# Optimization experiments

Measured on AMD Instinct MI355X. Metric: run time of the kernel, lower is better.

Reference implementation:

```python
import jax, jax.numpy as jnp
import numpy as np

N = 50000      # nodes
E = 1000000    # edges
B = 512        # graphs in batch
F = 32         # num_node_features
D = 64         # hidden_dim1
ED = 16        # edge_dim (8 edge_attr + 8 edge_feature)
STEPS = 3      # set2set processing steps


def setup_inputs() -> dict:
    key = jax.random.key(0)
    ks = jax.random.split(key, 24)
    rn = lambda k, shp, s=0.05: jax.random.normal(k, shp, dtype=jnp.float32) * s
    z = lambda *shp: jnp.zeros(shp, jnp.float32)
    inp = {}
    inp["x"] = jax.random.normal(ks[0], (N, F), dtype=jnp.float32)
    inp["edge_attr"] = jax.random.normal(ks[1], (E, 8), dtype=jnp.float32)
    inp["edge_feature"] = jax.random.normal(ks[2], (E, 8), dtype=jnp.float32)
    inp["edge_index"] = jax.random.randint(ks[3], (2, E), 0, N, dtype=jnp.int32)
    inp["batch"] = jnp.sort(jax.random.randint(ks[4], (N,), 0, B, dtype=jnp.int32))
    # conv0: GINEConv with nn = Linear(F,D)-ReLU-Linear(D,D); edge lin: ED -> F
    inp["conv0_ew"] = rn(ks[5], (ED, F)); inp["conv0_eb"] = z(F)
    inp["conv0_w1"] = rn(ks[6], (F, D));  inp["conv0_b1"] = z(D)
    inp["conv0_w2"] = rn(ks[7], (D, D));  inp["conv0_b2"] = z(D)
    # conv1: nn = Linear(D,D)-ReLU-Linear(D,D); edge lin: ED -> D
    inp["conv1_ew"] = rn(ks[8], (ED, D)); inp["conv1_eb"] = z(D)
    inp["conv1_w1"] = rn(ks[9], (D, D));  inp["conv1_b1"] = z(D)
    inp["conv1_w2"] = rn(ks[10], (D, D)); inp["conv1_b2"] = z(D)
    # Set2Set LSTM: input 2D -> hidden D (torch gate order i,f,g,o)
    inp["lstm_wih"] = rn(ks[11], (4 * D, 2 * D)); inp["lstm_bih"] = z(4 * D)
    inp["lstm_whh"] = rn(ks[12], (4 * D, D));     inp["lstm_bhh"] = z(4 * D)
    # dense head
    inp["dense_w"] = rn(ks[13], (2 * D, D)); inp["dense_b"] = z(D)
    inp["out_w"] = rn(ks[14], (D, 1));       inp["out_b"] = z(1)
    return inp


def _gine_conv(x, src, dst, eattr, ew, eb, w1, b1, w2, b2):
    # message = relu(x_j + lin(edge_attr)); sum-aggregate at target; eps=0
    msg = jax.nn.relu(x[src] + eattr @ ew + eb)          # [E, C]
    agg = jax.ops.segment_sum(msg, dst, num_segments=N)   # [N, C]
    h = x + agg                                            # (1+eps)*x + agg, eps=0
    return jax.nn.relu(h @ w1 + b1) @ w2 + b2


def _set2set(x, batch, wih, whh, bih, bhh):
    d = x.shape[1]
    q_star = jnp.zeros((B, 2 * d), x.dtype)
    h = jnp.zeros((B, d), x.dtype)
    c = jnp.zeros((B, d), x.dtype)
    for _ in range(STEPS):
        gates = q_star @ wih.T + bih + h @ whh.T + bhh     # [B, 4d]
        i, f, g, o = jnp.split(gates, 4, axis=1)
        c = jax.nn.sigmoid(f) * c + jax.nn.sigmoid(i) * jnp.tanh(g)
        h = jax.nn.sigmoid(o) * jnp.tanh(c)
        q = h                                              # [B, d]
        e = jnp.sum(x * q[batch], axis=-1)                 # [N]
        m = jax.ops.segment_max(e, batch, num_segments=B)
        ex = jnp.exp(e - m[batch])
        denom = jax.ops.segment_sum(ex, batch, num_segments=B)
        a = ex / denom[batch]                              # segmented softmax
        r = jax.ops.segment_sum(a[:, None] * x, batch, num_segments=B)  # [B, d]
        q_star = jnp.concatenate([q, r], axis=-1)
    return q_star


def reference(x, edge_attr, edge_feature, edge_index, batch,
              conv0_ew, conv0_eb, conv0_w1, conv0_b1, conv0_w2, conv0_b2,
              conv1_ew, conv1_eb, conv1_w1, conv1_b1, conv1_w2, conv1_b2,
              lstm_wih, lstm_whh, lstm_bih, lstm_bhh,
              dense_w, dense_b, out_w, out_b):
    ea = jnp.concatenate([edge_attr, edge_feature], axis=1)  # [E, ED]
    src, dst = edge_index[0], edge_index[1]
    h = jax.nn.relu(_gine_conv(x, src, dst, ea, conv0_ew, conv0_eb,
                               conv0_w1, conv0_b1, conv0_w2, conv0_b2))
    h = jax.nn.relu(_gine_conv(h, src, dst, ea, conv1_ew, conv1_eb,
                               conv1_w1, conv1_b1, conv1_w2, conv1_b2))
    pooled = _set2set(h, batch, lstm_wih, lstm_whh, lstm_bih, lstm_bhh)  # [B, 2D]
    z = jax.nn.relu(pooled @ dense_w + dense_b)
    return (z @ out_w + out_b)[:, 0]
```

## Files before the change

### kernel.cpp

```cpp
#include <hip/hip_runtime.h>
#include <math.h>

#define NN 50000
#define EE 1000000
#define BB 512

typedef _Float16 hf;
typedef __attribute__((ext_vector_type(2))) _Float16 hf2;

__device__ __forceinline__ float sigmoidf_(float x) { return 1.0f / (1.0f + __expf(-x)); }

__device__ __forceinline__ int uloadi(const int* p) {
    return __builtin_amdgcn_readfirstlane(*p);
}
__device__ __forceinline__ unsigned uloadu(const unsigned* p) {
    return (unsigned)__builtin_amdgcn_readfirstlane((int)*p);
}

__device__ __forceinline__ unsigned pack2(float a, float b) {
    hf2 h; h.x = (_Float16)a; h.y = (_Float16)b;
    return __builtin_bit_cast(unsigned, h);
}

__device__ __forceinline__ float dot2acc(unsigned au, hf2 w, float acc) {
    hf2 a = __builtin_bit_cast(hf2, au);
#if __has_builtin(__builtin_amdgcn_fdot2)
    return __builtin_amdgcn_fdot2(a, w, acc, false);
#else
    return acc + (float)a.x * (float)w.x + (float)a.y * (float)w.y;
#endif
}

__global__ __launch_bounds__(256) void setup_kernel(
    const int* __restrict__ batch, int* __restrict__ brow,
    const float* __restrict__ wih, const float* __restrict__ whh,
    float* __restrict__ wihT, float* __restrict__ whhT,
    int* __restrict__ counts, const float* __restrict__ x, unsigned* __restrict__ xh)
{
    int i = blockIdx.x * 256 + threadIdx.x;
    if (i < NN) {
        counts[i] = 0;
        int bi = batch[i];
        int prev = (i == 0) ? -1 : batch[i - 1];
        for (int v = prev + 1; v <= bi; ++v) brow[v] = i;
        if (i == NN - 1) for (int v = bi + 1; v <= BB; ++v) brow[v] = NN;
    }
    if (i < 128 * 256) wihT[i] = wih[(i & 255) * 128 + (i >> 8)];
    if (i < 64 * 256)  whhT[i] = whh[(i & 255) * 64 + (i >> 8)];
    if (i < NN * 8) {
        float4 v = reinterpret_cast<const float4*>(x)[i];
        uint2 o; o.x = pack2(v.x, v.y); o.y = pack2(v.z, v.w);
        reinterpret_cast<uint2*>(xh)[i] = o;
    }
}

__global__ __launch_bounds__(256) void rank_kernel(const int* __restrict__ ei,
                                                   int* __restrict__ counts,
                                                   int* __restrict__ rnk)
{
    int e = blockIdx.x * 256 + threadIdx.x;
    if (e < EE) rnk[e] = atomicAdd(&counts[ei[EE + e]], 1);
}

__global__ __launch_bounds__(1024) void scan_kernel(const int* __restrict__ counts,
                                                    int* __restrict__ rowptr)
{
    __shared__ int s[1024];
    int t = threadIdx.x;
    const int CH = (NN + 1023) / 1024;
    int lo = t * CH, hi = lo + CH < NN ? lo + CH : NN;
    int sum = 0;
    for (int i = lo; i < hi; ++i) sum += counts[i];
    s[t] = sum;
    __syncthreads();
    for (int off = 1; off < 1024; off <<= 1) {
        int v = (t >= off) ? s[t - off] : 0;
        __syncthreads();
        s[t] += v;
        __syncthreads();
    }
    int base = (t > 0) ? s[t - 1] : 0;
    for (int i = lo; i < hi; ++i) { rowptr[i] = base; base += counts[i]; }
    if (t == 1023) rowptr[NN] = s[1023];
}

__global__ __launch_bounds__(256) void pack_kernel(
    const int* __restrict__ ei, const int* __restrict__ rnk,
    const int* __restrict__ rowptr,
    const float* __restrict__ eattr, const float* __restrict__ efeat,
    int* __restrict__ srcp, unsigned* __restrict__ eah)
{
    int e = blockIdx.x * 256 + threadIdx.x;
    if (e >= EE) return;
    int pos = rowptr[ei[EE + e]] + rnk[e];
    srcp[pos] = ei[e];
    const float4* pa = reinterpret_cast<const float4*>(eattr) + (size_t)e * 2;
    const float4* pf = reinterpret_cast<const float4*>(efeat) + (size_t)e * 2;
    float4 v0 = pa[0], v1 = pa[1], v2 = pf[0], v3 = pf[1];
    uint4 o0, o1;
    o0.x = pack2(v0.x, v0.y); o0.y = pack2(v0.z, v0.w);
    o0.z = pack2(v1.x, v1.y); o0.w = pack2(v1.z, v1.w);
    o1.x = pack2(v2.x, v2.y); o1.y = pack2(v2.z, v2.w);
    o1.z = pack2(v3.x, v3.y); o1.w = pack2(v3.z, v3.w);
    uint4* o = reinterpret_cast<uint4*>(eah + (size_t)pos * 8);
    o[0] = o0; o[1] = o1;
}

__global__ __launch_bounds__(256) void gine32_kernel(
    const hf* __restrict__ xin, const int* __restrict__ pidx,
    const int* __restrict__ rowptr, const unsigned* __restrict__ eah,
    const float* __restrict__ ew, const float* __restrict__ eb,
    const float* __restrict__ w1, const float* __restrict__ b1,
    const float* __restrict__ w2, const float* __restrict__ b2,
    hf* __restrict__ hout)
{
    __shared__ float w1_lds[32 * 64];
    for (int i = threadIdx.x; i < 32 * 64; i += 256) w1_lds[i] = w1[i];
    __syncthreads();

    int wave = threadIdx.x >> 6, lane = threadIdx.x & 63;
    int node = blockIdx.x * 4 + wave;
    if (node >= NN) return;

    int ch = lane & 31;
    int half = lane >> 5;

    hf2 wh[8];
#pragma unroll
    for (int k = 0; k < 8; ++k) {
        wh[k].x = (_Float16)ew[(2 * k) * 32 + ch];
        wh[k].y = (_Float16)ew[(2 * k + 1) * 32 + ch];
    }
    float ebv = eb[ch];

    int start = rowptr[node], end = rowptr[node + 1];
    float agg = 0.0f;

    int j = start;
    for (; j + 1 < end; j += 2) {
        int jb = __builtin_amdgcn_readfirstlane(j);
        int s0 = uloadi(pidx + jb);
        int s1 = uloadi(pidx + jb + 1);
        float xv = (float)xin[(size_t)(half ? s1 : s0) * 32 + ch];
        const unsigned* p = eah + (size_t)jb * 8;
        unsigned a0[8], a1[8];
#pragma unroll
        for (int k = 0; k < 8; ++k) { a0[k] = uloadu(p + k); a1[k] = uloadu(p + 8 + k); }
        float m0 = 0.0f, m1 = 0.0f;
#pragma unroll
        for (int k = 0; k < 8; ++k) {
            m0 = dot2acc(a0[k], wh[k], m0);
            m1 = dot2acc(a1[k], wh[k], m1);
        }
        agg += fmaxf(xv + (half ? m1 : m0) + ebv, 0.0f);
    }
    if (j < end) {
        int jb = __builtin_amdgcn_readfirstlane(j);
        int s0 = uloadi(pidx + jb);
        float xv = (float)xin[(size_t)s0 * 32 + ch];
        const unsigned* p = eah + (size_t)jb * 8;
        float m0 = 0.0f;
#pragma unroll
        for (int k = 0; k < 8; ++k) m0 = dot2acc(uloadu(p + k), wh[k], m0);
        agg += (half == 0) ? fmaxf(xv + m0 + ebv, 0.0f) : 0.0f;
    }
    agg += __shfl_xor(agg, 32);

    float h_in = 0.0f;
    if (lane < 32) h_in = (float)xin[(size_t)node * 32 + lane] + agg;

    float hid = b1[lane];
#pragma unroll
    for (int i = 0; i < 32; ++i)
        hid += __shfl(h_in, i) * w1_lds[i * 64 + lane];
    hid = fmaxf(hid, 0.0f);

    float o = b2[lane];
#pragma unroll
    for (int i = 0; i < 64; ++i)
        o += __shfl(hid, i) * w2[i * 64 + lane];

    hout[(size_t)node * 64 + lane] = (hf)fmaxf(o, 0.0f);
}

__global__ __launch_bounds__(256) void gine64_kernel(
    const hf* __restrict__ xin, const int* __restrict__ pidx,
    const int* __restrict__ rowptr, const unsigned* __restrict__ eah,
    const float* __restrict__ ew, const float* __restrict__ eb,
    const float* __restrict__ w1, const float* __restrict__ b1,
    const float* __restrict__ w2, const float* __restrict__ b2,
    hf* __restrict__ hout)
{
    __shared__ float w1_lds[64 * 64];
    for (int i = threadIdx.x; i < 64 * 64; i += 256) w1_lds[i] = w1[i];
    __syncthreads();

    int wave = threadIdx.x >> 6, lane = threadIdx.x & 63;
    int node = blockIdx.x * 4 + wave;
    if (node >= NN) return;

    int ch32 = lane & 31;
    int half = lane >> 5;
    int start = rowptr[node], end = rowptr[node + 1];

    auto run_pass = [&](int cb) -> float {
        int c = cb + ch32;
        hf2 wh[8];
#pragma unroll
        for (int k = 0; k < 8; ++k) {
            wh[k].x = (_Float16)ew[(2 * k) * 64 + c];
            wh[k].y = (_Float16)ew[(2 * k + 1) * 64 + c];
        }
        float ebv = eb[c];
        float agg = 0.0f;
        int j = start;
        for (; j + 1 < end; j += 2) {
            int jb = __builtin_amdgcn_readfirstlane(j);
            int s0 = uloadi(pidx + jb);
            int s1 = uloadi(pidx + jb + 1);
            float xv = (float)xin[(size_t)(half ? s1 : s0) * 64 + c];
            const unsigned* p = eah + (size_t)jb * 8;
            unsigned a0[8], a1[8];
#pragma unroll
            for (int k = 0; k < 8; ++k) { a0[k] = uloadu(p + k); a1[k] = uloadu(p + 8 + k); }
            float m0 = 0.0f, m1 = 0.0f;
#pragma unroll
            for (int k = 0; k < 8; ++k) {
                m0 = dot2acc(a0[k], wh[k], m0);
                m1 = dot2acc(a1[k], wh[k], m1);
            }
            agg += fmaxf(xv + (half ? m1 : m0) + ebv, 0.0f);
        }
        if (j < end) {
            int jb = __builtin_amdgcn_readfirstlane(j);
            int s0 = uloadi(pidx + jb);
            float xv = (float)xin[(size_t)s0 * 64 + c];
            const unsigned* p = eah + (size_t)jb * 8;
            float m0 = 0.0f;
#pragma unroll
            for (int k = 0; k < 8; ++k) m0 = dot2acc(uloadu(p + k), wh[k], m0);
            agg += (half == 0) ? fmaxf(xv + m0 + ebv, 0.0f) : 0.0f;
        }
        agg += __shfl_xor(agg, 32);
        return agg;
    };

    float agg_lo = run_pass(0);
    float agg_hi = run_pass(32);

    float h_in = (float)xin[(size_t)node * 64 + lane]
               + ((lane < 32) ? agg_lo : agg_hi);

    float hid = b1[lane];
#pragma unroll
    for (int i = 0; i < 64; ++i)
        hid += __shfl(h_in, i) * w1_lds[i * 64 + lane];
    hid = fmaxf(hid, 0.0f);

    float o = b2[lane];
#pragma unroll
    for (int i = 0; i < 64; ++i)
        o += __shfl(hid, i) * w2[i * 64 + lane];

    hout[(size_t)node * 64 + lane] = (hf)fmaxf(o, 0.0f);
}

__global__ __launch_bounds__(1024) void set2set_head_v3(
    const hf* __restrict__ h2, const int* __restrict__ brow,
    const float* __restrict__ wihT, const float* __restrict__ whhT,
    const float* __restrict__ bih, const float* __restrict__ bhh,
    const float* __restrict__ dw, const float* __restrict__ db,
    const float* __restrict__ ow, const float* __restrict__ ob,
    float* __restrict__ outp)
{
    int b = blockIdx.x, tid = threadIdx.x;
    int wv = tid >> 6, lane = tid & 63;
    __shared__ float qstar[128], hh[64], cc[64];
    __shared__ float gpart[4][256];
    __shared__ float redw[16][64];
    __shared__ float redm[16], reds[16];

    int start = brow[b], end = brow[b + 1];

    if (tid < 128) qstar[tid] = 0.0f;
    if (tid < 64) { hh[tid] = 0.0f; cc[tid] = 0.0f; }
    __syncthreads();

    for (int step = 0; step < 3; ++step) {
        {
            int p = tid >> 8, g = tid & 255;
            float acc = 0.0f;
            const float* wT = wihT + (size_t)(32 * p) * 256 + g;
#pragma unroll 8
            for (int k = 0; k < 32; ++k) acc += qstar[32 * p + k] * wT[(size_t)k * 256];
            const float* hT = whhT + (size_t)(16 * p) * 256 + g;
#pragma unroll 8
            for (int k = 0; k < 16; ++k) acc += hh[16 * p + k] * hT[(size_t)k * 256];
            gpart[p][g] = acc;
        }
        __syncthreads();
        if (tid < 64) {
            float gi = bih[tid]       + bhh[tid]       + gpart[0][tid]       + gpart[1][tid]       + gpart[2][tid]       + gpart[3][tid];
            float gf = bih[64 + tid]  + bhh[64 + tid]  + gpart[0][64 + tid]  + gpart[1][64 + tid]  + gpart[2][64 + tid]  + gpart[3][64 + tid];
            float gg = bih[128 + tid] + bhh[128 + tid] + gpart[0][128 + tid] + gpart[1][128 + tid] + gpart[2][128 + tid] + gpart[3][128 + tid];
            float go = bih[192 + tid] + bhh[192 + tid] + gpart[0][192 + tid] + gpart[1][192 + tid] + gpart[2][192 + tid] + gpart[3][192 + tid];
            float c = sigmoidf_(gf) * cc[tid] + sigmoidf_(gi) * tanhf(gg);
            cc[tid] = c;
            hh[tid] = sigmoidf_(go) * tanhf(c);
        }
        __syncthreads();

        float qv = hh[lane];
        float mw = -INFINITY, sw = 0.0f, rw = 0.0f;
        for (int n = start + wv; n < end; n += 16) {
            float v = (float)h2[(size_t)n * 64 + lane];
            float p = v * qv;
#pragma unroll
            for (int off = 32; off; off >>= 1) p += __shfl_xor(p, off);
            float nm = fmaxf(mw, p);
            float sc = __expf(mw - nm);
            float pe = __expf(p - nm);
            sw = sw * sc + pe;
            rw = rw * sc + pe * v;
            mw = nm;
        }
        redm[wv] = mw; reds[wv] = sw; redw[wv][lane] = rw;
        __syncthreads();
        if (tid < 64) {
            float M = -INFINITY;
#pragma unroll
            for (int w = 0; w < 16; ++w) M = fmaxf(M, redm[w]);
            float S = 0.0f, R = 0.0f;
#pragma unroll
            for (int w = 0; w < 16; ++w) {
                float mm = redm[w];
                if (mm > -INFINITY) {
                    float sc = __expf(mm - M);
                    S += reds[w] * sc;
                    R += redw[w][tid] * sc;
                }
            }
            qstar[tid] = hh[tid];
            qstar[64 + tid] = (S > 0.0f) ? R / S : 0.0f;
        }
        __syncthreads();
    }

    if (tid < 64) {
        float z = db[tid];
#pragma unroll 4
        for (int k = 0; k < 128; ++k) z += qstar[k] * dw[k * 64 + tid];
        redw[0][tid] = fmaxf(z, 0.0f);
    }
    __syncthreads();
    if (tid < 64) {
        float t = redw[0][tid] * ow[tid];
#pragma unroll
        for (int off = 32; off; off >>= 1) t += __shfl_xor(t, off);
        if (tid == 0) outp[b] = t + ob[0];
    }
}

extern "C" void kernel_launch(void* const* d_in, const int* in_sizes, int n_in,
                              void* d_out, int out_size, void* d_ws, size_t ws_size,
                              hipStream_t stream)
{
    const float* x     = (const float*)d_in[0];
    const float* eattr = (const float*)d_in[1];
    const float* efeat = (const float*)d_in[2];
    const int*   ei    = (const int*)d_in[3];
    const int*   batch = (const int*)d_in[4];
    const float* c0_ew = (const float*)d_in[5];  const float* c0_eb = (const float*)d_in[6];
    const float* c0_w1 = (const float*)d_in[7];  const float* c0_b1 = (const float*)d_in[8];
    const float* c0_w2 = (const float*)d_in[9];  const float* c0_b2 = (const float*)d_in[10];
    const float* c1_ew = (const float*)d_in[11]; const float* c1_eb = (const float*)d_in[12];
    const float* c1_w1 = (const float*)d_in[13]; const float* c1_b1 = (const float*)d_in[14];
    const float* c1_w2 = (const float*)d_in[15]; const float* c1_b2 = (const float*)d_in[16];
    const float* wih   = (const float*)d_in[17]; const float* bih   = (const float*)d_in[18];
    const float* whh   = (const float*)d_in[19]; const float* bhh   = (const float*)d_in[20];
    const float* dw    = (const float*)d_in[21]; const float* dbias = (const float*)d_in[22];
    const float* ow    = (const float*)d_in[23]; const float* ob    = (const float*)d_in[24];

    float* out = (float*)d_out;
    int* iws = (int*)d_ws;

    int* counts = iws;
    int* rowptr = counts + NN;
    int* brow   = rowptr + NN + 1;
    size_t off0 = ((size_t)2 * NN + 1 + (BB + 1) + 15) & ~(size_t)15;
    float* wihT = (float*)(iws + off0);
    float* whhT = wihT + 128 * 256;
    int*   srcp = (int*)(whhT + 64 * 256);
    unsigned* xh = (unsigned*)(srcp + EE);
    size_t offE = (off0 + 128 * 256 + 64 * 256 + EE + (size_t)NN * 16 + 15) & ~(size_t)15;
    unsigned* eah = (unsigned*)(iws + offE);
    hf* h1h = (hf*)(eah + (size_t)EE * 8);
    hf* h2h = h1h + (size_t)NN * 64;
    int* rnk = (int*)h1h;

    int setup_grid = (NN * 8 + 255) / 256;
    setup_kernel<<<setup_grid, 256, 0, stream>>>(batch, brow, wih, whh,
                                                 wihT, whhT, counts, x, xh);
    rank_kernel<<<(EE + 255) / 256, 256, 0, stream>>>(ei, counts, rnk);
    scan_kernel<<<1, 1024, 0, stream>>>(counts, rowptr);
    pack_kernel<<<(EE + 255) / 256, 256, 0, stream>>>(
        ei, rnk, rowptr, eattr, efeat, srcp, eah);
    gine32_kernel<<<(NN + 3) / 4, 256, 0, stream>>>(
        (const hf*)xh, srcp, rowptr, eah,
        c0_ew, c0_eb, c0_w1, c0_b1, c0_w2, c0_b2, h1h);
    gine64_kernel<<<(NN + 3) / 4, 256, 0, stream>>>(
        h1h, srcp, rowptr, eah,
        c1_ew, c1_eb, c1_w1, c1_b1, c1_w2, c1_b2, h2h);
    set2set_head_v3<<<BB, 1024, 0, stream>>>(h2h, brow, wihT, whhT, bih, bhh,
                                             dw, dbias, ow, ob, out);
}
```

Before: 416.2 us.

## Process 4 edges per iteration and use full 64-lane channels in gine64

The 64-channel GINE kernel used two sequential 32-channel passes over each node's edge list, each lane-half handling a different edge. It now makes a single pass with all 64 lanes mapped to the 64 channels, so edge attributes and source indices are read once per edge instead of twice. Both GINE kernels also gain a 4-edge unrolled loop that puts more independent loads and dot products in flight. The cost is more registers per thread, which could lower occupancy.

```diff
diff --git a/kernel.cpp b/kernel.cpp
--- a/kernel.cpp
+++ b/kernel.cpp
@@ -137,6 +137,32 @@
     float agg = 0.0f;
 
     int j = start;
+    for (; j + 3 < end; j += 4) {
+        int jb = __builtin_amdgcn_readfirstlane(j);
+        int s0 = uloadi(pidx + jb),     s1 = uloadi(pidx + jb + 1);
+        int s2 = uloadi(pidx + jb + 2), s3 = uloadi(pidx + jb + 3);
+        float xva = (float)xin[(size_t)(half ? s1 : s0) * 32 + ch];
+        float xvb = (float)xin[(size_t)(half ? s3 : s2) * 32 + ch];
+        const unsigned* p = eah + (size_t)jb * 8;
+        unsigned a0[8], a1[8], a2[8], a3[8];
+#pragma unroll
+        for (int k = 0; k < 8; ++k) {
+            a0[k] = uloadu(p + k);
+            a1[k] = uloadu(p + 8 + k);
+            a2[k] = uloadu(p + 16 + k);
+            a3[k] = uloadu(p + 24 + k);
+        }
+        float m0 = 0.0f, m1 = 0.0f, m2 = 0.0f, m3 = 0.0f;
+#pragma unroll
+        for (int k = 0; k < 8; ++k) {
+            m0 = dot2acc(a0[k], wh[k], m0);
+            m1 = dot2acc(a1[k], wh[k], m1);
+            m2 = dot2acc(a2[k], wh[k], m2);
+            m3 = dot2acc(a3[k], wh[k], m3);
+        }
+        agg += fmaxf(xva + (half ? m1 : m0) + ebv, 0.0f)
+             + fmaxf(xvb + (half ? m3 : m2) + ebv, 0.0f);
+    }
     for (; j + 1 < end; j += 2) {
         int jb = __builtin_amdgcn_readfirstlane(j);
         int s0 = uloadi(pidx + jb);
@@ -199,57 +225,56 @@
     int node = blockIdx.x * 4 + wave;
     if (node >= NN) return;
 
-    int ch32 = lane & 31;
-    int half = lane >> 5;
+    hf2 wh[8];
+#pragma unroll
+    for (int k = 0; k < 8; ++k) {
+        wh[k].x = (_Float16)ew[(2 * k) * 64 + lane];
+        wh[k].y = (_Float16)ew[(2 * k + 1) * 64 + lane];
+    }
+    float ebv = eb[lane];
+
     int start = rowptr[node], end = rowptr[node + 1];
-
-    auto run_pass = [&](int cb) -> float {
-        int c = cb + ch32;
-        hf2 wh[8];
+    float agg = 0.0f;
+
+    int j = start;
+    for (; j + 3 < end; j += 4) {
+        int jb = __builtin_amdgcn_readfirstlane(j);
+        int s0 = uloadi(pidx + jb),     s1 = uloadi(pidx + jb + 1);
+        int s2 = uloadi(pidx + jb + 2), s3 = uloadi(pidx + jb + 3);
+        float m0 = (float)xin[(size_t)s0 * 64 + lane] + ebv;
+        float m1 = (float)xin[(size_t)s1 * 64 + lane] + ebv;
+        float m2 = (float)xin[(size_t)s2 * 64 + lane] + ebv;
+        float m3 = (float)xin[(size_t)s3 * 64 + lane] + ebv;
+        const unsigned* p = eah + (size_t)jb * 8;
+        unsigned a0[8], a1[8], a2[8], a3[8];
 #pragma unroll
         for (int k = 0; k < 8; ++k) {
-            wh[k].x = (_Float16)ew[(2 * k) * 64 + c];
-            wh[k].y = (_Float16)ew[(2 * k + 1) * 64 + c];
-        }
-        float ebv = eb[c];
-        float agg = 0.0f;
-        int j = start;
-        for (; j + 1 < end; j += 2) {
-            int jb = __builtin_amdgcn_readfirstlane(j);
-            int s0 = uloadi(pidx + jb);
-            int s1 = uloadi(pidx + jb + 1);
-            float xv = (float)xin[(size_t)(half ? s1 : s0) * 64 + c];
-            const unsigned* p = eah + (size_t)jb * 8;
-            unsigned a0[8], a1[8];
-#pragma unroll
-            for (int k = 0; k < 8; ++k) { a0[k] = uloadu(p + k); a1[k] = uloadu(p + 8 + k); }
-            float m0 = 0.0f, m1 = 0.0f;
-#pragma unroll
-            for (int k = 0; k < 8; ++k) {
-                m0 = dot2acc(a0[k], wh[k], m0);
-                m1 = dot2acc(a1[k], wh[k], m1);
-            }
-            agg += fmaxf(xv + (half ? m1 : m0) + ebv, 0.0f);
-        }
-        if (j < end) {
-            int jb = __builtin_amdgcn_readfirstlane(j);
-            int s0 = uloadi(pidx + jb);
-            float xv = (float)xin[(size_t)s0 * 64 + c];
-            const unsigned* p = eah + (size_t)jb * 8;
-            float m0 = 0.0f;
-#pragma unroll
-            for (int k = 0; k < 8; ++k) m0 = dot2acc(uloadu(p + k), wh[k], m0);
-            agg += (half == 0) ? fmaxf(xv + m0 + ebv, 0.0f) : 0.0f;
-        }
-        agg += __shfl_xor(agg, 32);
-        return agg;
-    };
-
-    float agg_lo = run_pass(0);
-    float agg_hi = run_pass(32);
-
-    float h_in = (float)xin[(size_t)node * 64 + lane]
-               + ((lane < 32) ? agg_lo : agg_hi);
+            a0[k] = uloadu(p + k);
+            a1[k] = uloadu(p + 8 + k);
+            a2[k] = uloadu(p + 16 + k);
+            a3[k] = uloadu(p + 24 + k);
+        }
+#pragma unroll
+        for (int k = 0; k < 8; ++k) {
+            m0 = dot2acc(a0[k], wh[k], m0);
+            m1 = dot2acc(a1[k], wh[k], m1);
+            m2 = dot2acc(a2[k], wh[k], m2);
+            m3 = dot2acc(a3[k], wh[k], m3);
+        }
+        agg += fmaxf(m0, 0.0f) + fmaxf(m1, 0.0f)
+             + fmaxf(m2, 0.0f) + fmaxf(m3, 0.0f);
+    }
+    for (; j < end; ++j) {
+        int jb = __builtin_amdgcn_readfirstlane(j);
+        int s0 = uloadi(pidx + jb);
+        float m0 = (float)xin[(size_t)s0 * 64 + lane] + ebv;
+        const unsigned* p = eah + (size_t)jb * 8;
+#pragma unroll
+        for (int k = 0; k < 8; ++k) m0 = dot2acc(uloadu(p + k), wh[k], m0);
+        agg += fmaxf(m0, 0.0f);
+    }
+
+    float h_in = (float)xin[(size_t)node * 64 + lane] + agg;
 
     float hid = b1[lane];
 #pragma unroll
```

New measurement: 379.0 us (median of 2 runs). 8.9% less time.
